# Kernel optimization log

Hardware: AMD Instinct MI355X
Metric: run time of the kernel (lower is better)

## Reference

```python
import jax, jax.numpy as jnp
import numpy as np

B, N, D = 4, 1024, 1024
H, DH = 16, 64
N_LAYERS = 3  # len(mlp_dims) - 1 with implicit_mlp_hiddens=(64, 64)
EPS = 1.1920929e-07  # torch.nn.RMSNorm default eps = finfo(float32).eps


def _rope_tables(n, dtype):
    # lucidrains RotaryEmbedding: theta=10000, interleaved freq repeat
    inv_freq = 1.0 / (10000.0 ** (np.arange(0, DH, 2, dtype=np.float64) / DH))
    t = np.arange(n, dtype=np.float64)[:, None] * inv_freq[None, :]  # [n, DH/2]
    t = np.repeat(t, 2, axis=-1)  # [n, DH], freqs interleaved (f0,f0,f1,f1,...)
    return jnp.asarray(np.cos(t), dtype), jnp.asarray(np.sin(t), dtype)


def _rope_rotate(x, cos, sin):
    # x: [b,h,n,d]; rotate_half on interleaved pairs: (x1,x2) -> (-x2,x1)
    xp = x.reshape(*x.shape[:-1], DH // 2, 2)
    xr = jnp.stack((-xp[..., 1], xp[..., 0]), axis=-1).reshape(x.shape)
    return x * cos + xr * sin


def _attend(q, k, v):
    # rotate_queries_with_cached_keys with no cache: same positions for q and k
    n = q.shape[-2]
    cos, sin = _rope_tables(n, q.dtype)
    q = _rope_rotate(q, cos, sin)
    k = _rope_rotate(k, cos, sin)
    scale = DH ** -0.5
    scores = jnp.einsum('bhqd,bhkd->bhqk', q, k) * scale
    causal = jnp.tril(jnp.ones((n, n), dtype=bool))
    scores = jnp.where(causal, scores, -jnp.inf)
    attn = jax.nn.softmax(scores, axis=-1)
    return jnp.einsum('bhqk,bhkd->bhqd', attn, v)


def _split_heads(x):
    b, n, _ = x.shape
    return x.reshape(b, n, H, DH).transpose(0, 2, 1, 3)  # b h n d


def setup_inputs() -> dict:
    key = jax.random.key(0)
    ks = jax.random.split(key, 6)
    s = 0.02
    return {
        'tokens': jax.random.normal(ks[0], (B, N, D), jnp.float32),
        'gamma': jnp.ones((D,), jnp.float32),                                  # RMSNorm weight
        'Wq': jax.random.normal(ks[1], (D, H * DH), jnp.float32) * s,           # to_queries
        'Wk': jax.random.normal(ks[2], (N_LAYERS, D, H * DH), jnp.float32) * s, # stacked key projections
        'Wv': jax.random.normal(ks[3], (N_LAYERS, D, H * DH), jnp.float32) * s, # stacked value projections
        'Wo': jax.random.normal(ks[4], (H * DH, D), jnp.float32) * s,           # to_out
    }


def reference(tokens, gamma, Wq, Wk, Wv, Wo):
    b, n, d = tokens.shape
    # RMSNorm (prenorm)
    x = tokens * jax.lax.rsqrt(jnp.mean(tokens * tokens, axis=-1, keepdims=True) + EPS) * gamma
    out = _split_heads(x @ Wq)  # queries, [b h n d]
    for i in range(N_LAYERS):
        k = _split_heads(x @ Wk[i])
        v = _split_heads(x @ Wv[i])
        out = _attend(out, k, v)
        if i < N_LAYERS - 1:
            out = jax.nn.silu(out)  # implicit MLP activation between attention stages
    out = out.transpose(0, 2, 1, 3).reshape(b, n, H * DH)  # merge heads
    return out @ Wo
```

## Files before the change

kernel.cpp:

```cpp
#include <hip/hip_runtime.h>


typedef unsigned short u16;
typedef short s16x8 __attribute__((ext_vector_type(8)));
typedef u16 u16x4 __attribute__((ext_vector_type(4)));
typedef float f32x4 __attribute__((ext_vector_type(4)));

typedef __attribute__((address_space(1))) const unsigned int as1c_uint;
typedef __attribute__((address_space(3))) unsigned int as3_uint;

__device__ __forceinline__ float b2f(u16 h) {
  union { unsigned int u; float f; } v; v.u = ((unsigned int)h) << 16; return v.f;
}
__device__ __forceinline__ u16 f2b(float f) {
  union { float f; unsigned int u; } v; v.f = f;
  return (u16)((v.u + 0x7FFFu + ((v.u >> 16) & 1u)) >> 16);
}
__device__ __forceinline__ void gload16(const u16* g, const u16* lds) {
  __builtin_amdgcn_global_load_lds((as1c_uint*)(size_t)g,
                                   (as3_uint*)(unsigned int)(size_t)lds, 16, 0, 0);
}

__global__ __launch_bounds__(256)
void rmsnorm_kernel(const float* __restrict__ T, const float* __restrict__ gamma,
                    u16* __restrict__ X) {
  const int row = blockIdx.x, tid = threadIdx.x;
  const float4 v = ((const float4*)(T + (size_t)row * 1024))[tid];
  float ss = v.x * v.x + v.y * v.y + v.z * v.z + v.w * v.w;
#pragma unroll
  for (int msk = 1; msk <= 32; msk <<= 1) ss += __shfl_xor(ss, msk, 64);
  __shared__ float red[4];
  if ((tid & 63) == 0) red[tid >> 6] = ss;
  __syncthreads();
  const float tot = red[0] + red[1] + red[2] + red[3];
  const float r = rsqrtf(tot * (1.0f / 1024.0f) + 1.1920929e-07f);
  const float4 gm = ((const float4*)gamma)[tid];
  u16x4 o;
  o[0] = f2b(v.x * r * gm.x); o[1] = f2b(v.y * r * gm.y);
  o[2] = f2b(v.z * r * gm.z); o[3] = f2b(v.w * r * gm.w);
  *(u16x4*)(X + (size_t)row * 1024 + tid * 4) = o;
}

__global__ __launch_bounds__(256)
void rope_kernel(float* __restrict__ ct, float* __restrict__ st) {
  const int idx = blockIdx.x * 256 + threadIdx.x;
  const int n = idx >> 5, j = idx & 31;
  const double freq = pow(10000.0, -(double)j / 32.0);
  const double a = (double)n * freq;
  ct[idx] = (float)cos(a);
  st[idx] = (float)sin(a);
}

__global__ __launch_bounds__(256)
void transw_kernel(const float* __restrict__ Wq, const float* __restrict__ Wk,
                   const float* __restrict__ Wv, const float* __restrict__ Wo,
                   u16* __restrict__ wt) {
  __shared__ float tile[32][33];
  const int z = blockIdx.z;
  const float* src = (z == 0) ? Wq
                   : (z <= 3) ? (Wk + (size_t)(z - 1) * 1048576)
                   : (z <= 6) ? (Wv + (size_t)(z - 4) * 1048576)
                              : Wo;
  u16* dst = wt + (size_t)z * 1048576;
  const int tx = threadIdx.x & 31, ty = threadIdx.x >> 5;
  const int bx = blockIdx.x * 32, by = blockIdx.y * 32;
#pragma unroll
  for (int i = 0; i < 4; ++i)
    tile[ty + i * 8][tx] = src[(size_t)(by + ty + i * 8) * 1024 + bx + tx];
  __syncthreads();
#pragma unroll
  for (int i = 0; i < 4; ++i)
    dst[(size_t)(bx + ty + i * 8) * 1024 + by + tx] = f2b(tile[tx][ty + i * 8]);
}

template <int KIND>
__global__ __launch_bounds__(256, 2)
void gemm_kernel(const u16* __restrict__ A, const u16* __restrict__ Bt,
                 void* __restrict__ Cout, const float* __restrict__ ct,
                 const float* __restrict__ st) {
  constexpr int MB = (KIND == 0) ? 8 : 4;
  constexpr int BM = MB * 32;
  constexpr int ASLOT = BM * 32;
  constexpr int SLOT = (BM + 128) * 32;
  const int p = blockIdx.x;
  const int role = (p & 7) * (KIND == 0 ? 112 : 64) + (p >> 3);
  const int z = (KIND == 0) ? (role >> 7) : (role >> 8);
  const int rem = (KIND == 0) ? (role & 127) : (role & 255);
  const int m0 = (rem >> 3) * BM;
  const int n0 = (rem & 7) * 128;

  const int tid = threadIdx.x;
  const int w = tid >> 6, l = tid & 63;
  const int g = l >> 4, ll = l & 15;
  const int wr = w >> 1, wc = w & 1;

  const u16* Ab;
  const u16* Bb;
  if (KIND == 0) {
    Ab = A + (size_t)m0 * 1024;
    Bb = Bt + (size_t)z * 1048576 + (size_t)n0 * 1024;
  } else {
    Ab = A + (size_t)m0 * 1024 + z * 512;
    Bb = Bt + (size_t)n0 * 1024 + z * 512;
  }

  __shared__ u16 SH[3][SLOT];

  const f32x4 zero = {0.f, 0.f, 0.f, 0.f};
  f32x4 acc[MB][4];
#pragma unroll
  for (int i = 0; i < MB; ++i)
#pragma unroll
    for (int j = 0; j < 4; ++j) acc[i][j] = zero;

  auto stage = [&](int t2) {
    const int slot = t2 % 3;
    const int k0 = t2 * 32;
    const int rsub = l >> 2, sl = l & 3;
#pragma unroll
    for (int c = 0; c < MB / 2; ++c) {
      const int chunk = c * 4 + w;
      const int row = chunk * 16 + rsub;
      const int kk = k0 + ((sl ^ ((row >> 1) & 3)) << 3);
      gload16(Ab + (size_t)row * 1024 + kk, &SH[slot][chunk * 512]);
    }
#pragma unroll
    for (int c = 0; c < 2; ++c) {
      const int chunk = c * 4 + w;
      const int row = chunk * 16 + rsub;
      const int kk = k0 + ((sl ^ ((row >> 1) & 3)) << 3);
      gload16(Bb + (size_t)row * 1024 + kk, &SH[slot][ASLOT + chunk * 512]);
    }
  };

  const int NT = (KIND == 1) ? 16 : 32;
  stage(0); stage(1);

#pragma unroll
  for (int t = 0; t < NT; ++t) {
    if (t < NT - 1) {
      if constexpr (KIND == 0) asm volatile("s_waitcnt vmcnt(6)" ::: "memory");
      else                     asm volatile("s_waitcnt vmcnt(4)" ::: "memory");
    } else {
      asm volatile("s_waitcnt vmcnt(0)" ::: "memory");
    }
    __builtin_amdgcn_s_barrier();

    const int slot = t % 3;
    const u16* As = &SH[slot][0];
    const u16* Bs = &SH[slot][ASLOT];
    s16x8 bfr[4];
#pragma unroll
    for (int nf = 0; nf < 4; ++nf) {
      const int row = wc * 64 + nf * 16 + ll;
      bfr[nf] = *(const s16x8*)&Bs[row * 32 + ((g ^ ((row >> 1) & 3)) << 3)];
    }
    s16x8 af[MB];
#pragma unroll
    for (int mf = 0; mf < MB; ++mf) {
      const int row = wr * (MB * 16) + mf * 16 + ll;
      af[mf] = *(const s16x8*)&As[row * 32 + ((g ^ ((row >> 1) & 3)) << 3)];
    }

    if (t + 2 < NT) stage(t + 2);

    __builtin_amdgcn_s_setprio(1);
#pragma unroll
    for (int mf = 0; mf < MB; ++mf)
#pragma unroll
      for (int nf = 0; nf < 4; ++nf)
        acc[mf][nf] = __builtin_amdgcn_mfma_f32_16x16x32_bf16(af[mf], bfr[nf],
                                                              acc[mf][nf], 0, 0, 0);
    __builtin_amdgcn_s_setprio(0);
  }
  __syncthreads();

  if (KIND == 0) {
    u16* C = (u16*)Cout + (size_t)z * 4194304;
    if (z < 4) {
      const bool doRope = (z >= 1);
      u16* T = &SH[0][0];
#pragma unroll
      for (int mf = 0; mf < MB; ++mf)
#pragma unroll
        for (int nf = 0; nf < 4; ++nf) {
          const int c = wc * 64 + nf * 16 + ll;
#pragma unroll
          for (int rg = 0; rg < 4; ++rg) {
            const int r = wr * (MB * 16) + mf * 16 + g * 4 + rg;
            T[r * 128 + (c ^ ((r & 7) << 4))] = f2b(acc[mf][nf][rg]);
          }
        }
      __syncthreads();
#pragma unroll
      for (int i = 0; i < BM / 16; ++i) {
        const int R = (tid >> 4) + i * 16;
        const int c0 = (tid & 15) * 8;
        s16x8 v = *(const s16x8*)&T[R * 128 + (c0 ^ ((R & 7) << 4))];
        if (doRope) {
          const int n = (m0 + R) & 1023;
          const int j0 = (c0 & 63) >> 1;
          const float4 c4 = *(const float4*)(ct + n * 32 + j0);
          const float4 s4 = *(const float4*)(st + n * 32 + j0);
          s16x8 vo;
#pragma unroll
          for (int pp = 0; pp < 4; ++pp) {
            const float c = ((const float*)&c4)[pp];
            const float s = ((const float*)&s4)[pp];
            const float x0 = b2f((u16)v[2 * pp]), x1 = b2f((u16)v[2 * pp + 1]);
            vo[2 * pp]     = (short)f2b(x0 * c - x1 * s);
            vo[2 * pp + 1] = (short)f2b(x1 * c + x0 * s);
          }
          v = vo;
        }
        *(s16x8*)&C[(size_t)(m0 + R) * 1024 + n0 + c0] = v;
      }
    } else {
#pragma unroll
      for (int mf = 0; mf < MB; ++mf)
#pragma unroll
        for (int nf = 0; nf < 4; ++nf) {
          const int col = n0 + wc * 64 + nf * 16 + ll;
          const int hh = col >> 6, d = col & 63;
          const int mb = m0 + wr * (MB * 16) + mf * 16 + g * 4;
          const int bb = mb >> 10, n = mb & 1023;
          u16x4 pk;
#pragma unroll
          for (int rg = 0; rg < 4; ++rg) pk[rg] = f2b(acc[mf][nf][rg]);
          *(u16x4*)&C[((size_t)((bb * 16 + hh) * 64 + d)) * 1024 + n] = pk;
        }
    }
  } else {
    float* C = (float*)Cout + (size_t)z * 4194304;
#pragma unroll
    for (int mf = 0; mf < MB; ++mf)
#pragma unroll
      for (int nf = 0; nf < 4; ++nf) {
        const int col = n0 + wc * 64 + nf * 16 + ll;
#pragma unroll
        for (int rg = 0; rg < 4; ++rg) {
          const int m = m0 + wr * (MB * 16) + mf * 16 + g * 4 + rg;
          C[(size_t)m * 1024 + col] = acc[mf][nf][rg];
        }
      }
  }
}

__global__ __launch_bounds__(256)
void reduce_kernel(const float* __restrict__ P, float* __restrict__ out) {
  const int i = (blockIdx.x * 256 + threadIdx.x) * 4;
  const float4 a = *(const float4*)(P + i);
  const float4 b = *(const float4*)(P + 4194304 + i);
  float4 o;
  o.x = a.x + b.x; o.y = a.y + b.y; o.z = a.z + b.z; o.w = a.w + b.w;
  *(float4*)(out + i) = o;
}

template <int SILU>
__global__ __launch_bounds__(256)
void attn_kernel(const u16* __restrict__ Q, const u16* __restrict__ K,
                 const u16* __restrict__ Vt, u16* __restrict__ O,
                 const float* __restrict__ ct, const float* __restrict__ st) {
  const int lin = blockIdx.x + (blockIdx.y << 3);
  const int role = (lin & 7) * 64 + (lin >> 3);
  const int p = role & 7, bh = role >> 3;
  const int q_lo = p, q_hi = 15 - p;
  const int b = bh >> 4, h = bh & 15;
  const int tid = threadIdx.x, w = tid >> 6, l = tid & 63;
  const int g = l >> 4, ll = l & 15;

  const u16* Qb = Q + (size_t)(b * 1024) * 1024 + h * 64;
  const u16* Kb = K + (size_t)(b * 1024) * 1024 + h * 64;
  const u16* Vb = Vt + (size_t)((b * 16 + h) * 64) * 1024;
  u16* Ob = O + (size_t)(b * 1024) * 1024 + h * 64;

  __shared__ u16 Ksh[2][64 * 72];
  __shared__ u16 Psh[4][16 * 72];

  s16x8 qfL[2], qfH[2];
  auto loadQ = [&](int qt, s16x8* qf) {
    const int qrow = qt * 64 + w * 16 + ll;
#pragma unroll
    for (int kc = 0; kc < 2; ++kc) {
      const int d0 = kc * 32 + g * 8;
      const int j0 = d0 >> 1;
      const float4 c4 = *(const float4*)(ct + qrow * 32 + j0);
      const float4 s4v = *(const float4*)(st + qrow * 32 + j0);
      const s16x8 qin = *(const s16x8*)(Qb + (size_t)qrow * 1024 + d0);
      s16x8 qo;
#pragma unroll
      for (int pp = 0; pp < 4; ++pp) {
        const float c = ((const float*)&c4)[pp], s = ((const float*)&s4v)[pp];
        const float x0 = b2f((u16)qin[2 * pp]), x1 = b2f((u16)qin[2 * pp + 1]);
        qo[2 * pp]     = (short)f2b((x0 * c - x1 * s) * 0.125f);
        qo[2 * pp + 1] = (short)f2b((x1 * c + x0 * s) * 0.125f);
      }
      qf[kc] = qo;
    }
  };
  loadQ(q_lo, qfL);
  loadQ(q_hi, qfH);

  float lsL[4], lsH[4];
  f32x4 oL[4], oH[4];
  const f32x4 zero = {0.f, 0.f, 0.f, 0.f};
#pragma unroll
  for (int rg = 0; rg < 4; ++rg) { lsL[rg] = 0.f; lsH[rg] = 0.f; }
#pragma unroll
  for (int df = 0; df < 4; ++df) { oL[df] = zero; oH[df] = zero; }

  const int srow = tid >> 2;
  const int sc0 = (tid & 3) * 16;

  s16x8 kr0, kr1;
  auto kload = [&](int t) {
    const u16* kp = Kb + (size_t)(t * 64 + srow) * 1024 + sc0;
    kr0 = *(const s16x8*)kp;
    kr1 = *(const s16x8*)(kp + 8);
  };
  auto kstore = [&](int bf) {
    *(s16x8*)&Ksh[bf][srow * 72 + sc0] = kr0;
    *(s16x8*)&Ksh[bf][srow * 72 + sc0 + 8] = kr1;
  };

  kload(0);
  kstore(0);
  __syncthreads();
  int buf = 0;

  for (int t = 0; t <= q_hi; ++t) {
    const bool pre = (t < q_hi);
    if (pre) kload(t + 1);

    s16x8 vb[2][4];
#pragma unroll
    for (int kc = 0; kc < 2; ++kc)
#pragma unroll
      for (int df = 0; df < 4; ++df)
        vb[kc][df] = *(const s16x8*)(Vb + (size_t)(df * 16 + ll) * 1024 +
                                     t * 64 + kc * 32 + g * 8);

    auto process = [&](const s16x8* qf, float* ls, f32x4* o, bool diag) {
      f32x4 s4[4];
      __builtin_amdgcn_s_setprio(1);
#pragma unroll
      for (int nf = 0; nf < 4; ++nf) {
        const s16x8 kb0 = *(const s16x8*)&Ksh[buf][(nf * 16 + ll) * 72 + g * 8];
        const s16x8 kb1 = *(const s16x8*)&Ksh[buf][(nf * 16 + ll) * 72 + 32 + g * 8];
        f32x4 sv = zero;
        sv = __builtin_amdgcn_mfma_f32_16x16x32_bf16(qf[0], kb0, sv, 0, 0, 0);
        sv = __builtin_amdgcn_mfma_f32_16x16x32_bf16(qf[1], kb1, sv, 0, 0, 0);
        s4[nf] = sv;
      }
      __builtin_amdgcn_s_setprio(0);

      if (diag) {
#pragma unroll
        for (int nf = 0; nf < 4; ++nf)
#pragma unroll
          for (int rg = 0; rg < 4; ++rg)
            if (nf * 16 + ll > w * 16 + g * 4 + rg) s4[nf][rg] = -3.0e38f;
      }

#pragma unroll
      for (int rg = 0; rg < 4; ++rg) {
        float ps = 0.f;
#pragma unroll
        for (int nf = 0; nf < 4; ++nf) {
          const float pv = __expf(s4[nf][rg] - 12.f);
          s4[nf][rg] = pv;
          ps += pv;
        }
        ls[rg] += ps;
      }

#pragma unroll
      for (int nf = 0; nf < 4; ++nf)
#pragma unroll
        for (int rg = 0; rg < 4; ++rg)
          Psh[w][(g * 4 + rg) * 72 + nf * 16 + ll] = f2b(s4[nf][rg]);

      __builtin_amdgcn_s_setprio(1);
#pragma unroll
      for (int kc = 0; kc < 2; ++kc) {
        const s16x8 pa = *(const s16x8*)&Psh[w][ll * 72 + kc * 32 + g * 8];
#pragma unroll
        for (int df = 0; df < 4; ++df)
          o[df] = __builtin_amdgcn_mfma_f32_16x16x32_bf16(pa, vb[kc][df],
                                                          o[df], 0, 0, 0);
      }
      __builtin_amdgcn_s_setprio(0);
    };

    process(qfH, lsH, oH, t == q_hi);
    if (t <= q_lo) process(qfL, lsL, oL, t == q_lo);

    if (pre) kstore(buf ^ 1);
    __syncthreads();
    buf ^= 1;
  }

  auto finish = [&](float* ls, f32x4* o, int qt) {
#pragma unroll
    for (int rg = 0; rg < 4; ++rg) {
      float v = ls[rg];
      v += __shfl_xor(v, 1, 64);
      v += __shfl_xor(v, 2, 64);
      v += __shfl_xor(v, 4, 64);
      v += __shfl_xor(v, 8, 64);
      ls[rg] = 1.f / v;
    }
#pragma unroll
    for (int df = 0; df < 4; ++df)
#pragma unroll
      for (int rg = 0; rg < 4; ++rg) {
        float val = o[df][rg] * ls[rg];
        if (SILU) val = val / (1.f + __expf(-val));
        Ob[(size_t)(qt * 64 + w * 16 + g * 4 + rg) * 1024 + df * 16 + ll] =
            f2b(val);
      }
  };
  finish(lsH, oH, q_hi);
  finish(lsL, oL, q_lo);
}

extern "C" void kernel_launch(void* const* d_in, const int* in_sizes, int n_in,
                              void* d_out, int out_size, void* d_ws, size_t ws_size,
                              hipStream_t stream) {
  (void)in_sizes; (void)n_in; (void)out_size; (void)ws_size;
  const float* tokens = (const float*)d_in[0];
  const float* gamma  = (const float*)d_in[1];
  const float* Wq     = (const float*)d_in[2];
  const float* Wk     = (const float*)d_in[3];
  const float* Wv     = (const float*)d_in[4];
  const float* Wo     = (const float*)d_in[5];
  float* out = (float*)d_out;

  u16* x    = (u16*)d_ws;
  u16* wt   = x + (size_t)4096 * 1024;
  u16* qkv  = wt + (size_t)8 * 1048576;
  u16* outA = qkv + (size_t)7 * 4194304;
  u16* outB = outA + 4194304;
  float* ct = (float*)(outB + 4194304);
  float* st = ct + 32768;
  float* Pp = (float*)(qkv + 1 * 4194304);

  rmsnorm_kernel<<<4096, 256, 0, stream>>>(tokens, gamma, x);
  rope_kernel<<<128, 256, 0, stream>>>(ct, st);
  transw_kernel<<<dim3(32, 32, 8), 256, 0, stream>>>(Wq, Wk, Wv, Wo, wt);
  gemm_kernel<0><<<896, 256, 0, stream>>>(x, wt, qkv, ct, st);

  const size_t M4 = 4194304;
  attn_kernel<1><<<dim3(8, 64), 256, 0, stream>>>(qkv, qkv + 1 * M4, qkv + 4 * M4,
                                                  outA, ct, st);
  attn_kernel<1><<<dim3(8, 64), 256, 0, stream>>>(outA, qkv + 2 * M4, qkv + 5 * M4,
                                                  outB, ct, st);
  attn_kernel<0><<<dim3(8, 64), 256, 0, stream>>>(outB, qkv + 3 * M4, qkv + 6 * M4,
                                                  outA, ct, st);

  gemm_kernel<1><<<512, 256, 0, stream>>>(outA, wt + (size_t)7 * 1048576,
                                          (void*)Pp, ct, st);
  reduce_kernel<<<4096, 256, 0, stream>>>(Pp, out);
}
```

Baseline: 229.5 us.

## Process 128-key tiles per attention iteration and widen weight transpose tiles

The attention loop now stages two 64-key blocks (128 rows) of K in LDS per iteration and loads V for both sub-blocks, halving the number of barrier-synchronised iterations and K staging rounds. The weight transpose kernel uses 64x64 tiles with float4 loads and 4-wide bf16 stores in place of scalar 32x32 tiles. The larger K buffer raises LDS use and the doubled V register fragments raise register pressure, which may lower occupancy. When q_hi is even, the last iteration also loads K rows one tile past the causal limit that are never used.

```diff
diff --git a/kernel.cpp b/kernel.cpp
--- a/kernel.cpp
+++ b/kernel.cpp
@@ -55,22 +55,34 @@
 void transw_kernel(const float* __restrict__ Wq, const float* __restrict__ Wk,
                    const float* __restrict__ Wv, const float* __restrict__ Wo,
                    u16* __restrict__ wt) {
-  __shared__ float tile[32][33];
+  __shared__ float tile[64][65];
   const int z = blockIdx.z;
   const float* src = (z == 0) ? Wq
                    : (z <= 3) ? (Wk + (size_t)(z - 1) * 1048576)
                    : (z <= 6) ? (Wv + (size_t)(z - 4) * 1048576)
                               : Wo;
   u16* dst = wt + (size_t)z * 1048576;
-  const int tx = threadIdx.x & 31, ty = threadIdx.x >> 5;
-  const int bx = blockIdx.x * 32, by = blockIdx.y * 32;
-#pragma unroll
-  for (int i = 0; i < 4; ++i)
-    tile[ty + i * 8][tx] = src[(size_t)(by + ty + i * 8) * 1024 + bx + tx];
+  const int tid = threadIdx.x;
+  const int bx = blockIdx.x * 64;
+  const int by = blockIdx.y * 64;
+  const int tcol = (tid & 15) * 4, trow = tid >> 4;
+#pragma unroll
+  for (int i = 0; i < 4; ++i) {
+    const int r = trow + i * 16;
+    const float4 v = *(const float4*)(src + (size_t)(bx + r) * 1024 + by + tcol);
+    tile[r][tcol] = v.x; tile[r][tcol + 1] = v.y;
+    tile[r][tcol + 2] = v.z; tile[r][tcol + 3] = v.w;
+  }
   __syncthreads();
-#pragma unroll
-  for (int i = 0; i < 4; ++i)
-    dst[(size_t)(bx + ty + i * 8) * 1024 + by + tx] = f2b(tile[tx][ty + i * 8]);
+  const int k4 = (tid & 15) * 4;
+#pragma unroll
+  for (int j = 0; j < 4; ++j) {
+    const int R = (tid >> 4) + j * 16;
+    u16x4 o;
+    o[0] = f2b(tile[k4][R]);     o[1] = f2b(tile[k4 + 1][R]);
+    o[2] = f2b(tile[k4 + 2][R]); o[3] = f2b(tile[k4 + 3][R]);
+    *(u16x4*)&dst[(size_t)(by + R) * 1024 + bx + k4] = o;
+  }
 }
 
 template <int KIND>
@@ -274,7 +286,7 @@
   const u16* Vb = Vt + (size_t)((b * 16 + h) * 64) * 1024;
   u16* Ob = O + (size_t)(b * 1024) * 1024 + h * 64;
 
-  __shared__ u16 Ksh[2][64 * 72];
+  __shared__ u16 Ksh[2][128 * 72];
   __shared__ u16 Psh[4][16 * 72];
 
   s16x8 qfL[2], qfH[2];
@@ -312,15 +324,20 @@
   const int srow = tid >> 2;
   const int sc0 = (tid & 3) * 16;
 
-  s16x8 kr0, kr1;
-  auto kload = [&](int t) {
-    const u16* kp = Kb + (size_t)(t * 64 + srow) * 1024 + sc0;
+  s16x8 kr0, kr1, kr2, kr3;
+  auto kload = [&](int tt) {
+    const u16* kp = Kb + (size_t)(tt * 128 + srow) * 1024 + sc0;
     kr0 = *(const s16x8*)kp;
     kr1 = *(const s16x8*)(kp + 8);
+    const u16* kp2 = kp + (size_t)64 * 1024;
+    kr2 = *(const s16x8*)kp2;
+    kr3 = *(const s16x8*)(kp2 + 8);
   };
   auto kstore = [&](int bf) {
     *(s16x8*)&Ksh[bf][srow * 72 + sc0] = kr0;
     *(s16x8*)&Ksh[bf][srow * 72 + sc0 + 8] = kr1;
+    *(s16x8*)&Ksh[bf][(64 + srow) * 72 + sc0] = kr2;
+    *(s16x8*)&Ksh[bf][(64 + srow) * 72 + sc0 + 8] = kr3;
   };
 
   kload(0);
@@ -328,25 +345,30 @@
   __syncthreads();
   int buf = 0;
 
-  for (int t = 0; t <= q_hi; ++t) {
-    const bool pre = (t < q_hi);
-    if (pre) kload(t + 1);
-
-    s16x8 vb[2][4];
-#pragma unroll
-    for (int kc = 0; kc < 2; ++kc)
-#pragma unroll
-      for (int df = 0; df < 4; ++df)
-        vb[kc][df] = *(const s16x8*)(Vb + (size_t)(df * 16 + ll) * 1024 +
-                                     t * 64 + kc * 32 + g * 8);
-
-    auto process = [&](const s16x8* qf, float* ls, f32x4* o, bool diag) {
+  const int iters = (q_hi + 2) >> 1;
+  for (int tt = 0; tt < iters; ++tt) {
+    const bool pre = (tt + 1 < iters);
+    if (pre) kload(tt + 1);
+
+    s16x8 vb[2][2][4];
+#pragma unroll
+    for (int sub = 0; sub < 2; ++sub)
+#pragma unroll
+      for (int kc = 0; kc < 2; ++kc)
+#pragma unroll
+        for (int df = 0; df < 4; ++df)
+          vb[sub][kc][df] = *(const s16x8*)(Vb + (size_t)(df * 16 + ll) * 1024 +
+                                           (tt * 2 + sub) * 64 + kc * 32 + g * 8);
+
+    auto process = [&](const s16x8* qf, float* ls, f32x4* o, int sub,
+                       bool diag) {
+      const int rb = sub * 64;
       f32x4 s4[4];
       __builtin_amdgcn_s_setprio(1);
 #pragma unroll
       for (int nf = 0; nf < 4; ++nf) {
-        const s16x8 kb0 = *(const s16x8*)&Ksh[buf][(nf * 16 + ll) * 72 + g * 8];
-        const s16x8 kb1 = *(const s16x8*)&Ksh[buf][(nf * 16 + ll) * 72 + 32 + g * 8];
+        const s16x8 kb0 = *(const s16x8*)&Ksh[buf][(rb + nf * 16 + ll) * 72 + g * 8];
+        const s16x8 kb1 = *(const s16x8*)&Ksh[buf][(rb + nf * 16 + ll) * 72 + 32 + g * 8];
         f32x4 sv = zero;
         sv = __builtin_amdgcn_mfma_f32_16x16x32_bf16(qf[0], kb0, sv, 0, 0, 0);
         sv = __builtin_amdgcn_mfma_f32_16x16x32_bf16(qf[1], kb1, sv, 0, 0, 0);
@@ -386,14 +408,17 @@
         const s16x8 pa = *(const s16x8*)&Psh[w][ll * 72 + kc * 32 + g * 8];
 #pragma unroll
         for (int df = 0; df < 4; ++df)
-          o[df] = __builtin_amdgcn_mfma_f32_16x16x32_bf16(pa, vb[kc][df],
+          o[df] = __builtin_amdgcn_mfma_f32_16x16x32_bf16(pa, vb[sub][kc][df],
                                                           o[df], 0, 0, 0);
       }
       __builtin_amdgcn_s_setprio(0);
     };
 
-    process(qfH, lsH, oH, t == q_hi);
-    if (t <= q_lo) process(qfL, lsL, oL, t == q_lo);
+    const int ka = 2 * tt, kb = 2 * tt + 1;
+    process(qfH, lsH, oH, 0, ka == q_hi);
+    if (kb <= q_hi) process(qfH, lsH, oH, 1, kb == q_hi);
+    if (ka <= q_lo) process(qfL, lsL, oL, 0, ka == q_lo);
+    if (kb <= q_lo) process(qfL, lsL, oL, 1, kb == q_lo);
 
     if (pre) kstore(buf ^ 1);
     __syncthreads();
@@ -447,7 +472,7 @@
 
   rmsnorm_kernel<<<4096, 256, 0, stream>>>(tokens, gamma, x);
   rope_kernel<<<128, 256, 0, stream>>>(ct, st);
-  transw_kernel<<<dim3(32, 32, 8), 256, 0, stream>>>(Wq, Wk, Wv, Wo, wt);
+  transw_kernel<<<dim3(16, 16, 8), 256, 0, stream>>>(Wq, Wk, Wv, Wo, wt);
   gemm_kernel<0><<<896, 256, 0, stream>>>(x, wt, qkv, ct, st);
 
   const size_t M4 = 4194304;
```

Result: no change. 228.8 us (-0.3%).
